# Kernel tuning notes

Measured on AMD Instinct MI355X. Metric: run time of the kernel, lower is better.

The kernel has to match this reference:

```python
import jax, jax.numpy as jnp
import numpy as np

# Static DAG configuration (mirrors GraphState): 1 input node + L layers of K nodes.
L = 8          # depth layers (well under t_budget=12)
K = 8          # nodes per layer
D = 128        # node hidden width (node.D)
B = 4096       # batch size
INDEG = 4      # in-edges per non-input node
N = 1 + L * K  # total nodes


def _build_graph():
    """Deterministic static edge lists: srcs[l][k, j] = parent node id (topologically earlier)."""
    rng = np.random.default_rng(0)
    srcs = []
    n_prev = 1  # node 0 is the INPUT node
    for _ in range(L):
        srcs.append(rng.integers(0, n_prev, size=(K, INDEG)))
        n_prev += K
    return srcs


def setup_inputs() -> dict:
    key = jax.random.key(0)
    k1, k2, k3 = jax.random.split(key, 3)
    X = jax.random.normal(k1, (B, D), dtype=jnp.float32)
    # scale ~ sqrt(2/(indeg*D)) to keep relu activations O(1) over 8 layers
    W = jax.random.normal(k2, (N, D, D), dtype=jnp.float32) * 0.06
    b = jax.random.normal(k3, (N, D), dtype=jnp.float32) * 0.01
    return {"X_batch": X, "W_all": W, "bias_all": b}


def reference(X_batch, W_all, bias_all):
    srcs = _build_graph()  # static python/numpy index constants -> jit-friendly
    # INPUT node (id 0): input_dim == D so no zero-padding; V_out = relu(X W^T + b)
    v0 = jax.nn.relu(X_batch @ W_all[0].T + bias_all[0])          # (B, D)
    outs = v0[None]                                               # (n_done, B, D)
    node = 1
    for l in range(L):
        idx = srcs[l]                                             # (K, INDEG) static
        V_in = outs[idx].sum(axis=1)                              # inbox gather-sum -> (K, B, D)
        Wl = W_all[node:node + K]                                 # (K, D, D)
        bl = bias_all[node:node + K]                              # (K, D)
        V_weighted = jnp.einsum('kbd,ked->kbe', V_in, Wl) + bl[:, None, :]
        V_out = jax.nn.relu(V_weighted)                           # apply_primitive(relu)
        outs = jnp.concatenate([outs, V_out], axis=0)
        node += K
    # output nodes = last layer; final = mean over fired output nodes
    return outs[-K:].mean(axis=0)                                 # (B, D)
```

## Files before the change

### kernel.cpp

```cpp
#include <hip/hip_runtime.h>
#include <cstdint>
#include <cstring>

#define BATCH   4096
#define DIM     128
#define NLAYERS 8
#define KNODES  8
#define NDEG    4
#define NNODES  65
#define NODE_ELEMS (BATCH * DIM)

typedef float    f32x4 __attribute__((ext_vector_type(4)));
typedef short    s16x8 __attribute__((ext_vector_type(8)));
typedef uint32_t u32x4 __attribute__((ext_vector_type(4)));

struct LayerSrcs { int p[KNODES][NDEG]; };

__device__ __forceinline__ float bf_lo(uint32_t u) {
  union { uint32_t i; float f; } x; x.i = u << 16; return x.f;
}
__device__ __forceinline__ float bf_hi(uint32_t u) {
  union { uint32_t i; float f; } x; x.i = u & 0xffff0000u; return x.f;
}
__device__ __forceinline__ uint32_t f2bf(float f) {
  union { float f; uint32_t i; } x; x.f = f;
  return (x.i + 0x7fffu + ((x.i >> 16) & 1u)) >> 16;
}
__device__ __forceinline__ uint32_t pack2(float a, float b) {
  return f2bf(a) | (f2bf(b) << 16);
}


__global__ __launch_bounds__(256)
void conv_w(const float* __restrict__ W, uint16_t* __restrict__ Wb) {
  size_t idx = ((size_t)blockIdx.x * 256 + threadIdx.x) * 8;
  f32x4 v0 = *(const f32x4*)(W + idx);
  f32x4 v1 = *(const f32x4*)(W + idx + 4);
  u32x4 pk;
  pk.x = pack2(v0.x, v0.y); pk.y = pack2(v0.z, v0.w);
  pk.z = pack2(v1.x, v1.y); pk.w = pack2(v1.z, v1.w);
  *(u32x4*)(Wb + idx) = pk;
}

template <int ROOT>
__global__ __launch_bounds__(256)
void node_gemm(const uint16_t* __restrict__ outs_r,
               uint16_t* __restrict__ outs_w,
               const uint16_t* __restrict__ Wb,
               const float* __restrict__ bias_all,
               const float* __restrict__ X,
               LayerSrcs srcs, int node_base)
{
  __shared__ char Alds[128 * 256];
  __shared__ char Blds[128 * 256];

  const int t = threadIdx.x;
  int k, tile;
  if (ROOT) { k = 0; tile = blockIdx.x; }
  else      { k = blockIdx.x & 7; tile = blockIdx.x >> 3; }
  const int node = node_base + k;
  const int row0 = tile * 128;

  const char* wsrc = (const char*)(Wb + (size_t)node * (DIM * DIM));

  const uint16_t* psrc[NDEG];
  if (!ROOT) {
#pragma unroll
    for (int p = 0; p < NDEG; ++p)
      psrc[p] = outs_r + (size_t)srcs.p[k][p] * NODE_ELEMS;
  }

#pragma unroll
  for (int it = 0; it < 8; ++it) {
    const int lin   = it * 256 + t;
    const int r     = lin >> 4;
    const int c0    = (lin & 15) << 3;
    const int lbyte = lin << 4;
    const int sbyte = lbyte ^ ((r & 7) << 4);

    float a0, a1, a2, a3, a4, a5, a6, a7;
    if (ROOT) {
      const float* xp = X + (size_t)(row0 + r) * DIM + c0;
      f32x4 v0 = *(const f32x4*)xp;
      f32x4 v1 = *(const f32x4*)(xp + 4);
      a0 = v0.x; a1 = v0.y; a2 = v0.z; a3 = v0.w;
      a4 = v1.x; a5 = v1.y; a6 = v1.z; a7 = v1.w;
    } else {
      a0 = a1 = a2 = a3 = a4 = a5 = a6 = a7 = 0.f;
#pragma unroll
      for (int p = 0; p < NDEG; ++p) {
        u32x4 v = *(const u32x4*)(psrc[p] + (size_t)(row0 + r) * DIM + c0);
        a0 += bf_lo(v.x); a1 += bf_hi(v.x);
        a2 += bf_lo(v.y); a3 += bf_hi(v.y);
        a4 += bf_lo(v.z); a5 += bf_hi(v.z);
        a6 += bf_lo(v.w); a7 += bf_hi(v.w);
      }
    }
    u32x4 pk;
    pk.x = pack2(a0, a1); pk.y = pack2(a2, a3);
    pk.z = pack2(a4, a5); pk.w = pack2(a6, a7);
    *(u32x4*)(Alds + sbyte) = pk;

    *(u32x4*)(Blds + sbyte) = *(const u32x4*)(wsrc + lbyte);
  }
  __syncthreads();

  const int lane = t & 63;
  const int w    = t >> 6;
  const int lr   = lane & 15;
  const int lg   = lane >> 4;

  f32x4 acc[2][8];
#pragma unroll
  for (int m = 0; m < 2; ++m)
#pragma unroll
    for (int n = 0; n < 8; ++n)
      acc[m][n] = (f32x4){0.f, 0.f, 0.f, 0.f};

#pragma unroll
  for (int ks = 0; ks < 4; ++ks) {
    const int kb = ks * 64 + lg * 16;
    s16x8 af[2], bfr[8];
#pragma unroll
    for (int m = 0; m < 2; ++m) {
      int r = w * 32 + m * 16 + lr;
      af[m] = *(const s16x8*)(Alds + ((r * 256 + kb) ^ ((r & 7) << 4)));
    }
#pragma unroll
    for (int n = 0; n < 8; ++n) {
      int e = n * 16 + lr;
      bfr[n] = *(const s16x8*)(Blds + ((e * 256 + kb) ^ ((e & 7) << 4)));
    }
#pragma unroll
    for (int m = 0; m < 2; ++m)
#pragma unroll
      for (int n = 0; n < 8; ++n)
        acc[m][n] = __builtin_amdgcn_mfma_f32_16x16x32_bf16(af[m], bfr[n], acc[m][n], 0, 0, 0);
  }

  uint16_t* dst = outs_w + (size_t)node * NODE_ELEMS;
  const float* bp = bias_all + (size_t)node * DIM;
#pragma unroll
  for (int n = 0; n < 8; ++n) {
    const int col = n * 16 + lr;
    const float bv = bp[col];
#pragma unroll
    for (int m = 0; m < 2; ++m) {
      const int rb = row0 + w * 32 + m * 16 + lg * 4;
#pragma unroll
      for (int j = 0; j < 4; ++j) {
        float v = fmaxf(acc[m][n][j] + bv, 0.f);
        dst[(size_t)(rb + j) * DIM + col] = (uint16_t)f2bf(v);
      }
    }
  }
}

__global__ __launch_bounds__(256)
void mean_last(const uint16_t* __restrict__ outs, float* __restrict__ out) {
  const size_t eoff = ((size_t)blockIdx.x * 256 + threadIdx.x) * 8;
  float a0 = 0, a1 = 0, a2 = 0, a3 = 0, a4 = 0, a5 = 0, a6 = 0, a7 = 0;
#pragma unroll
  for (int n = NNODES - KNODES; n < NNODES; ++n) {
    u32x4 v = *(const u32x4*)(outs + (size_t)n * NODE_ELEMS + eoff);
    a0 += bf_lo(v.x); a1 += bf_hi(v.x);
    a2 += bf_lo(v.y); a3 += bf_hi(v.y);
    a4 += bf_lo(v.z); a5 += bf_hi(v.z);
    a6 += bf_lo(v.w); a7 += bf_hi(v.w);
  }
  f32x4 o0 = {a0 * 0.125f, a1 * 0.125f, a2 * 0.125f, a3 * 0.125f};
  f32x4 o1 = {a4 * 0.125f, a5 * 0.125f, a6 * 0.125f, a7 * 0.125f};
  *(f32x4*)(out + eoff)     = o0;
  *(f32x4*)(out + eoff + 4) = o1;
}

namespace nprng {
static inline uint32_t hashmix(uint32_t v, uint32_t& hc) {
  v ^= hc; hc *= 0x931e8875u; v *= hc; v ^= v >> 16; return v;
}
static inline uint32_t mixf(uint32_t x, uint32_t y) {
  uint32_t r = x * 0xca01f9ddu - y * 0x4973f715u;
  r ^= r >> 16;
  return r;
}
struct Pcg {
  unsigned __int128 state, inc;
  bool has32; uint32_t saved;
  void step() {
    const unsigned __int128 MUL =
        ((unsigned __int128)2549297995355413924ULL << 64) | 4865540595714422341ULL;
    state = state * MUL + inc;
  }
  void init_seed0() {
    uint32_t pool[4];
    uint32_t hc = 0x43b0d7e5u;
    for (int i = 0; i < 4; ++i) pool[i] = hashmix(0u, hc);
    for (int s = 0; s < 4; ++s)
      for (int d = 0; d < 4; ++d)
        if (s != d) pool[d] = mixf(pool[d], hashmix(pool[s], hc));
    uint32_t st[8];
    uint32_t hb = 0x8b51f9ddu;
    int cyc = 0;
    for (int i = 0; i < 8; ++i) {
      uint32_t dv = pool[cyc]; cyc = (cyc + 1) & 3;
      dv ^= hb; hb *= 0x58f38dedu; dv *= hb; dv ^= dv >> 16;
      st[i] = dv;
    }
    uint64_t v[4];
    for (int i = 0; i < 4; ++i)
      v[i] = (uint64_t)st[2 * i] | ((uint64_t)st[2 * i + 1] << 32);
    unsigned __int128 s128 = ((unsigned __int128)v[0] << 64) | v[1];
    unsigned __int128 i128 = ((unsigned __int128)v[2] << 64) | v[3];
    state = 0; inc = (i128 << 1) | 1;
    step(); state += s128; step();
    has32 = false; saved = 0;
  }
  uint64_t next64() {
    step();
    uint64_t rot = (uint64_t)(state >> 122);
    uint64_t x = (uint64_t)(state >> 64) ^ (uint64_t)state;
    return rot ? ((x >> rot) | (x << (64 - rot))) : x;
  }
  uint32_t next32() {
    if (has32) { has32 = false; return saved; }
    uint64_t v = next64();
    has32 = true; saved = (uint32_t)(v >> 32);
    return (uint32_t)v;
  }
  uint32_t lemire32(uint32_t rng_incl) {
    uint32_t rng_excl = rng_incl + 1u;
    uint64_t m = (uint64_t)next32() * (uint64_t)rng_excl;
    uint32_t leftover = (uint32_t)m;
    if (leftover < rng_excl) {
      uint32_t threshold = (0xFFFFFFFFu - rng_incl) % rng_excl;
      while (leftover < threshold) {
        m = (uint64_t)next32() * (uint64_t)rng_excl;
        leftover = (uint32_t)m;
      }
    }
    return (uint32_t)(m >> 32);
  }
};
}

extern "C" void kernel_launch(void* const* d_in, const int* in_sizes, int n_in,
                              void* d_out, int out_size, void* d_ws, size_t ws_size,
                              hipStream_t stream) {
  const float* X    = (const float*)d_in[0];
  const float* W    = (const float*)d_in[1];
  const float* bias = (const float*)d_in[2];
  float* out        = (float*)d_out;

  uint16_t* Wb   = (uint16_t*)d_ws;
  uint16_t* outs = (uint16_t*)((char*)d_ws + (size_t)NNODES * DIM * DIM * 2);

  nprng::Pcg rng; rng.init_seed0();
  LayerSrcs srcs[NLAYERS];
  int n_prev = 1;
  for (int l = 0; l < NLAYERS; ++l) {
    for (int k = 0; k < KNODES; ++k)
      for (int j = 0; j < NDEG; ++j)
        srcs[l].p[k][j] = (n_prev == 1) ? 0 : (int)rng.lemire32((uint32_t)(n_prev - 1));
    n_prev += KNODES;
  }

  conv_w<<<dim3(520), dim3(256), 0, stream>>>(W, Wb);

  LayerSrcs zero{};
  node_gemm<1><<<dim3(32), dim3(256), 0, stream>>>(outs, outs, Wb, bias, X, zero, 0);

  for (int l = 0; l < NLAYERS; ++l) {
    node_gemm<0><<<dim3(256), dim3(256), 0, stream>>>(outs, outs, Wb, bias, nullptr,
                                                      srcs[l], 1 + l * KNODES);
  }

  mean_last<<<dim3(256), dim3(256), 0, stream>>>(outs, out);
}
```

Measured before the change: 138.5 us.

## Fuse whole DAG into one persistent kernel with LDS-resident node activations

Replaces the per-layer GEMM launches and the separate mean kernel with one kernel. Each block owns 16 batch rows and runs every layer, keeping live node activations in LDS slots assigned by a host-side liveness and slot allocator. The final mean is accumulated in registers. Nodes that do not reach the outputs are skipped, and weights are pre-packed into the MFMA fragment layout so they can be read straight from global memory. This removes launch overhead and the global round trips of intermediate activations. In exchange it uses a large LDS footprint (about 156KB) per block and reads weights redundantly in every block.

```diff
diff --git a/kernel.cpp b/kernel.cpp
--- a/kernel.cpp
+++ b/kernel.cpp
@@ -9,6 +9,10 @@
 #define NDEG    4
 #define NNODES  65
 #define NODE_ELEMS (BATCH * DIM)
+#define ROWS    16
+#define SLOTS   35
+#define TILE_B  (ROWS * 256)
+#define NTHREADS 512
 
 typedef float    f32x4 __attribute__((ext_vector_type(4)));
 typedef short    s16x8 __attribute__((ext_vector_type(8)));
@@ -16,6 +20,12 @@
 
 struct LayerSrcs { int p[KNODES][NDEG]; };
 
+struct Sched {
+  uint64_t pinfo[NLAYERS * KNODES];
+  int8_t   dst[NLAYERS * KNODES];
+  int8_t   root_dst;
+};
+
 __device__ __forceinline__ float bf_lo(uint32_t u) {
   union { uint32_t i; float f; } x; x.i = u << 16; return x.f;
 }
@@ -30,148 +40,211 @@
   return f2bf(a) | (f2bf(b) << 16);
 }
 
-
 __global__ __launch_bounds__(256)
-void conv_w(const float* __restrict__ W, uint16_t* __restrict__ Wb) {
-  size_t idx = ((size_t)blockIdx.x * 256 + threadIdx.x) * 8;
-  f32x4 v0 = *(const f32x4*)(W + idx);
-  f32x4 v1 = *(const f32x4*)(W + idx + 4);
+void pack_w(const float* __restrict__ W, uint16_t* __restrict__ Wp) {
+  int gid  = blockIdx.x * 256 + threadIdx.x;
+  int lane = gid & 63;
+  int n    = (gid >> 6) & 7;
+  int ks   = (gid >> 9) & 3;
+  int node = gid >> 11;
+  int col  = n * 16 + (lane & 15);
+  int k0   = ks * 32 + (lane >> 4) * 8;
+  const float* src = W + ((size_t)node * DIM + col) * DIM + k0;
+  f32x4 v0 = *(const f32x4*)src;
+  f32x4 v1 = *(const f32x4*)(src + 4);
   u32x4 pk;
   pk.x = pack2(v0.x, v0.y); pk.y = pack2(v0.z, v0.w);
   pk.z = pack2(v1.x, v1.y); pk.w = pack2(v1.z, v1.w);
-  *(u32x4*)(Wb + idx) = pk;
-}
-
-template <int ROOT>
-__global__ __launch_bounds__(256)
-void node_gemm(const uint16_t* __restrict__ outs_r,
-               uint16_t* __restrict__ outs_w,
-               const uint16_t* __restrict__ Wb,
-               const float* __restrict__ bias_all,
-               const float* __restrict__ X,
-               LayerSrcs srcs, int node_base)
+  *(u32x4*)(Wp + (size_t)gid * 8) = pk;
+}
+
+__device__ __forceinline__ void gemm_node(
+    char* lds, int sbuf, int n, int dstv,
+    const uint16_t* __restrict__ Wp, const float* __restrict__ bias,
+    uint16_t* __restrict__ outs, float* macc,
+    int row0, int lane, int w, int lr, int lg)
 {
-  __shared__ char Alds[128 * 256];
-  __shared__ char Blds[128 * 256];
-
-  const int t = threadIdx.x;
-  int k, tile;
-  if (ROOT) { k = 0; tile = blockIdx.x; }
-  else      { k = blockIdx.x & 7; tile = blockIdx.x >> 3; }
-  const int node = node_base + k;
-  const int row0 = tile * 128;
-
-  const char* wsrc = (const char*)(Wb + (size_t)node * (DIM * DIM));
-
-  const uint16_t* psrc[NDEG];
-  if (!ROOT) {
-#pragma unroll
-    for (int p = 0; p < NDEG; ++p)
-      psrc[p] = outs_r + (size_t)srcs.p[k][p] * NODE_ELEMS;
-  }
-
-#pragma unroll
-  for (int it = 0; it < 8; ++it) {
-    const int lin   = it * 256 + t;
-    const int r     = lin >> 4;
-    const int c0    = (lin & 15) << 3;
-    const int lbyte = lin << 4;
-    const int sbyte = lbyte ^ ((r & 7) << 4);
-
-    float a0, a1, a2, a3, a4, a5, a6, a7;
-    if (ROOT) {
-      const float* xp = X + (size_t)(row0 + r) * DIM + c0;
-      f32x4 v0 = *(const f32x4*)xp;
-      f32x4 v1 = *(const f32x4*)(xp + 4);
-      a0 = v0.x; a1 = v0.y; a2 = v0.z; a3 = v0.w;
-      a4 = v1.x; a5 = v1.y; a6 = v1.z; a7 = v1.w;
-    } else {
-      a0 = a1 = a2 = a3 = a4 = a5 = a6 = a7 = 0.f;
-#pragma unroll
-      for (int p = 0; p < NDEG; ++p) {
-        u32x4 v = *(const u32x4*)(psrc[p] + (size_t)(row0 + r) * DIM + c0);
-        a0 += bf_lo(v.x); a1 += bf_hi(v.x);
-        a2 += bf_lo(v.y); a3 += bf_hi(v.y);
-        a4 += bf_lo(v.z); a5 += bf_hi(v.z);
-        a6 += bf_lo(v.w); a7 += bf_hi(v.w);
-      }
-    }
-    u32x4 pk;
-    pk.x = pack2(a0, a1); pk.y = pack2(a2, a3);
-    pk.z = pack2(a4, a5); pk.w = pack2(a6, a7);
-    *(u32x4*)(Alds + sbyte) = pk;
-
-    *(u32x4*)(Blds + sbyte) = *(const u32x4*)(wsrc + lbyte);
-  }
-  __syncthreads();
-
+  if (dstv == -3) return;
+  const char* sb = lds + (size_t)(SLOTS + sbuf) * TILE_B;
+  s16x8 af[4], wf[4];
+#pragma unroll
+  for (int ks = 0; ks < 4; ++ks) {
+    af[ks] = *(const s16x8*)(sb + ((lr * 256 + ks * 64 + lg * 16) ^ ((lr & 7) << 4)));
+    wf[ks] = *(const s16x8*)(Wp + ((((size_t)n * 4 + ks) * 8 + w) << 9) + lane * 8);
+  }
+  f32x4 acc = (f32x4){0.f, 0.f, 0.f, 0.f};
+#pragma unroll
+  for (int ks = 0; ks < 4; ++ks)
+    acc = __builtin_amdgcn_mfma_f32_16x16x32_bf16(af[ks], wf[ks], acc, 0, 0, 0);
+
+  const int col = w * 16 + lr;
+  const float bv = bias[(size_t)n * DIM + col];
+  if (dstv >= 0) {
+    char* db = lds + (size_t)dstv * TILE_B;
+#pragma unroll
+    for (int j = 0; j < 4; ++j) {
+      int row = lg * 4 + j;
+      float v = fmaxf(acc[j] + bv, 0.f);
+      *(uint16_t*)(db + ((row * 256 + col * 2) ^ ((row & 7) << 4))) = (uint16_t)f2bf(v);
+    }
+  } else if (dstv == -1) {
+    uint16_t* gb = outs + (size_t)n * NODE_ELEMS + (size_t)row0 * DIM + col;
+#pragma unroll
+    for (int j = 0; j < 4; ++j) {
+      int row = lg * 4 + j;
+      float v = fmaxf(acc[j] + bv, 0.f);
+      gb[(size_t)row * DIM] = (uint16_t)f2bf(v);
+      gb += 0;
+    }
+  } else {
+#pragma unroll
+    for (int j = 0; j < 4; ++j)
+      macc[j] += 0.125f * fmaxf(acc[j] + bv, 0.f);
+  }
+}
+
+
+__device__ __forceinline__ void gemm_node2(
+    char* lds, int sbuf, int n, int dstv,
+    const uint16_t* __restrict__ Wp, const float* __restrict__ bias,
+    uint16_t* __restrict__ outs, float* macc,
+    int row0, int lane, int w, int lr, int lg)
+{
+  if (dstv == -3) return;
+  const char* sb = lds + (size_t)(SLOTS + sbuf) * TILE_B;
+  s16x8 af[4], wf[4];
+#pragma unroll
+  for (int ks = 0; ks < 4; ++ks) {
+    af[ks] = *(const s16x8*)(sb + ((lr * 256 + ks * 64 + lg * 16) ^ ((lr & 7) << 4)));
+    wf[ks] = *(const s16x8*)(Wp + ((((size_t)n * 4 + ks) * 8 + w) << 9) + lane * 8);
+  }
+  f32x4 acc = (f32x4){0.f, 0.f, 0.f, 0.f};
+#pragma unroll
+  for (int ks = 0; ks < 4; ++ks)
+    acc = __builtin_amdgcn_mfma_f32_16x16x32_bf16(af[ks], wf[ks], acc, 0, 0, 0);
+
+  const int col = w * 16 + lr;
+  const float bv = bias[(size_t)n * DIM + col];
+  if (dstv >= 0) {
+    char* db = lds + (size_t)dstv * TILE_B;
+#pragma unroll
+    for (int j = 0; j < 4; ++j) {
+      int row = lg * 4 + j;
+      float v = fmaxf(acc[j] + bv, 0.f);
+      *(uint16_t*)(db + ((row * 256 + col * 2) ^ ((row & 7) << 4))) = (uint16_t)f2bf(v);
+    }
+  } else if (dstv == -1) {
+    uint16_t* gb = outs + (size_t)n * NODE_ELEMS + (size_t)row0 * DIM + col;
+#pragma unroll
+    for (int j = 0; j < 4; ++j) {
+      int row = lg * 4 + j;
+      float v = fmaxf(acc[j] + bv, 0.f);
+      gb[(size_t)row * DIM] = (uint16_t)f2bf(v);
+    }
+  } else {
+#pragma unroll
+    for (int j = 0; j < 4; ++j)
+      macc[j] += 0.125f * fmaxf(acc[j] + bv, 0.f);
+  }
+}
+
+__global__ __launch_bounds__(NTHREADS)
+void dag_exec(const float* __restrict__ X, const uint16_t* __restrict__ Wp,
+              const float* __restrict__ bias, uint16_t* __restrict__ outs,
+              float* __restrict__ out, Sched sch)
+{
+  __shared__ char lds[(SLOTS + 4) * TILE_B];
+  const int t    = threadIdx.x;
   const int lane = t & 63;
   const int w    = t >> 6;
   const int lr   = lane & 15;
   const int lg   = lane >> 4;
-
-  f32x4 acc[2][8];
-#pragma unroll
-  for (int m = 0; m < 2; ++m)
-#pragma unroll
-    for (int n = 0; n < 8; ++n)
-      acc[m][n] = (f32x4){0.f, 0.f, 0.f, 0.f};
-
-#pragma unroll
-  for (int ks = 0; ks < 4; ++ks) {
-    const int kb = ks * 64 + lg * 16;
-    s16x8 af[2], bfr[8];
-#pragma unroll
-    for (int m = 0; m < 2; ++m) {
-      int r = w * 32 + m * 16 + lr;
-      af[m] = *(const s16x8*)(Alds + ((r * 256 + kb) ^ ((r & 7) << 4)));
-    }
-#pragma unroll
-    for (int n = 0; n < 8; ++n) {
-      int e = n * 16 + lr;
-      bfr[n] = *(const s16x8*)(Blds + ((e * 256 + kb) ^ ((e & 7) << 4)));
-    }
-#pragma unroll
-    for (int m = 0; m < 2; ++m)
-#pragma unroll
-      for (int n = 0; n < 8; ++n)
-        acc[m][n] = __builtin_amdgcn_mfma_f32_16x16x32_bf16(af[m], bfr[n], acc[m][n], 0, 0, 0);
-  }
-
-  uint16_t* dst = outs_w + (size_t)node * NODE_ELEMS;
-  const float* bp = bias_all + (size_t)node * DIM;
-#pragma unroll
-  for (int n = 0; n < 8; ++n) {
-    const int col = n * 16 + lr;
-    const float bv = bp[col];
-#pragma unroll
-    for (int m = 0; m < 2; ++m) {
-      const int rb = row0 + w * 32 + m * 16 + lg * 4;
-#pragma unroll
-      for (int j = 0; j < 4; ++j) {
-        float v = fmaxf(acc[m][n][j] + bv, 0.f);
-        dst[(size_t)(rb + j) * DIM + col] = (uint16_t)f2bf(v);
-      }
-    }
-  }
-}
-
-__global__ __launch_bounds__(256)
-void mean_last(const uint16_t* __restrict__ outs, float* __restrict__ out) {
-  const size_t eoff = ((size_t)blockIdx.x * 256 + threadIdx.x) * 8;
-  float a0 = 0, a1 = 0, a2 = 0, a3 = 0, a4 = 0, a5 = 0, a6 = 0, a7 = 0;
-#pragma unroll
-  for (int n = NNODES - KNODES; n < NNODES; ++n) {
-    u32x4 v = *(const u32x4*)(outs + (size_t)n * NODE_ELEMS + eoff);
-    a0 += bf_lo(v.x); a1 += bf_hi(v.x);
-    a2 += bf_lo(v.y); a3 += bf_hi(v.y);
-    a4 += bf_lo(v.z); a5 += bf_hi(v.z);
-    a6 += bf_lo(v.w); a7 += bf_hi(v.w);
-  }
-  f32x4 o0 = {a0 * 0.125f, a1 * 0.125f, a2 * 0.125f, a3 * 0.125f};
-  f32x4 o1 = {a4 * 0.125f, a5 * 0.125f, a6 * 0.125f, a7 * 0.125f};
-  *(f32x4*)(out + eoff)     = o0;
-  *(f32x4*)(out + eoff + 4) = o1;
+  const int row0 = blockIdx.x * ROWS;
+
+  float macc[4] = {0.f, 0.f, 0.f, 0.f};
+
+  if (t < ROWS * 16) {
+    int r = t >> 4, c = t & 15;
+    const float* xp = X + (size_t)(row0 + r) * DIM + c * 8;
+    f32x4 v0 = *(const f32x4*)xp;
+    f32x4 v1 = *(const f32x4*)(xp + 4);
+    u32x4 pk;
+    pk.x = pack2(v0.x, v0.y); pk.y = pack2(v0.z, v0.w);
+    pk.z = pack2(v1.x, v1.y); pk.w = pack2(v1.z, v1.w);
+    int off = (r * 256 + c * 16) ^ ((r & 7) << 4);
+    *(u32x4*)(lds + (size_t)SLOTS * TILE_B + off) = pk;
+  }
+  __syncthreads();
+  gemm_node2(lds, 0, 0, sch.root_dst, Wp, bias, outs, macc, row0, lane, w, lr, lg);
+  __syncthreads();
+
+  for (int l = 0; l < NLAYERS; ++l) {
+#pragma unroll
+    for (int h = 0; h < 2; ++h) {
+      const int k0 = h * 4;
+      const uint64_t pi0 = sch.pinfo[l * KNODES + k0 + 0];
+      const uint64_t pi1 = sch.pinfo[l * KNODES + k0 + 1];
+      const uint64_t pi2 = sch.pinfo[l * KNODES + k0 + 2];
+      const uint64_t pi3 = sch.pinfo[l * KNODES + k0 + 3];
+      const int d0 = sch.dst[l * KNODES + k0 + 0];
+      const int d1 = sch.dst[l * KNODES + k0 + 1];
+      const int d2 = sch.dst[l * KNODES + k0 + 2];
+      const int d3 = sch.dst[l * KNODES + k0 + 3];
+
+#pragma unroll
+      for (int it = 0; it < 2; ++it) {
+        const int lin = it * NTHREADS + t;
+        const int nk  = lin >> 8;
+        const uint64_t pinfo = (nk < 2) ? (nk == 0 ? pi0 : pi1) : (nk == 2 ? pi2 : pi3);
+        const int dv         = (nk < 2) ? (nk == 0 ? d0 : d1) : (nk == 2 ? d2 : d3);
+        if (dv != -3) {
+          const int r = (lin >> 4) & 15, c = lin & 15;
+          const int linoff = r * 256 + (c << 4);
+          const int soff   = linoff ^ ((r & 7) << 4);
+          float s0 = 0, s1 = 0, s2 = 0, s3 = 0, s4 = 0, s5 = 0, s6 = 0, s7 = 0;
+#pragma unroll
+          for (int p = 0; p < NDEG; ++p) {
+            const int e  = (int)((pinfo >> (p * 16)) & 0xffff);
+            const int ps = (e & 0xff) - 1;
+            u32x4 v;
+            if (ps >= 0) {
+              v = *(const u32x4*)(lds + (size_t)ps * TILE_B + soff);
+            } else {
+              const int pid = e >> 8;
+              v = *(const u32x4*)((const char*)(outs + (size_t)pid * NODE_ELEMS +
+                                                (size_t)row0 * DIM) + linoff);
+            }
+            s0 += bf_lo(v.x); s1 += bf_hi(v.x);
+            s2 += bf_lo(v.y); s3 += bf_hi(v.y);
+            s4 += bf_lo(v.z); s5 += bf_hi(v.z);
+            s6 += bf_lo(v.w); s7 += bf_hi(v.w);
+          }
+          u32x4 pk;
+          pk.x = pack2(s0, s1); pk.y = pack2(s2, s3);
+          pk.z = pack2(s4, s5); pk.w = pack2(s6, s7);
+          *(u32x4*)(lds + (size_t)(SLOTS + nk) * TILE_B + soff) = pk;
+        }
+      }
+      __syncthreads();
+
+#pragma unroll
+      for (int nk = 0; nk < 4; ++nk) {
+        const int dv = (nk < 2) ? (nk == 0 ? d0 : d1) : (nk == 2 ? d2 : d3);
+        const int n  = 1 + l * KNODES + k0 + nk;
+        gemm_node2(lds, nk, n, dv, Wp, bias, outs, macc, row0, lane, w, lr, lg);
+      }
+      __syncthreads();
+    }
+  }
+
+  {
+    const int col = w * 16 + lr;
+#pragma unroll
+    for (int j = 0; j < 4; ++j) {
+      const int row = lg * 4 + j;
+      out[(size_t)(row0 + row) * DIM + col] = macc[j];
+    }
+  }
 }
 
 namespace nprng {
@@ -251,7 +324,7 @@
   const float* bias = (const float*)d_in[2];
   float* out        = (float*)d_out;
 
-  uint16_t* Wb   = (uint16_t*)d_ws;
+  uint16_t* Wp   = (uint16_t*)d_ws;
   uint16_t* outs = (uint16_t*)((char*)d_ws + (size_t)NNODES * DIM * DIM * 2);
 
   nprng::Pcg rng; rng.init_seed0();
@@ -264,15 +337,58 @@
     n_prev += KNODES;
   }
 
-  conv_w<<<dim3(520), dim3(256), 0, stream>>>(W, Wb);
-
-  LayerSrcs zero{};
-  node_gemm<1><<<dim3(32), dim3(256), 0, stream>>>(outs, outs, Wb, bias, X, zero, 0);
+  bool alive[NNODES];
+  for (int i = 0; i < NNODES; ++i) alive[i] = false;
+  for (int i = NNODES - KNODES; i < NNODES; ++i) alive[i] = true;
+  for (int l = NLAYERS - 1; l >= 0; --l)
+    for (int k = 0; k < KNODES; ++k)
+      if (alive[1 + l * KNODES + k])
+        for (int j = 0; j < NDEG; ++j) alive[srcs[l].p[k][j]] = true;
+
+  int last_use[NNODES];
+  for (int i = 0; i < NNODES; ++i) last_use[i] = -1;
+  for (int l = 0; l < NLAYERS; ++l)
+    for (int k = 0; k < KNODES; ++k)
+      if (alive[1 + l * KNODES + k])
+        for (int j = 0; j < NDEG; ++j) {
+          int s = srcs[l].p[k][j];
+          if (l > last_use[s]) last_use[s] = l;
+        }
+
+  int slot_of[NNODES];
+  for (int i = 0; i < NNODES; ++i) slot_of[i] = -1;
+  int freeStk[SLOTS], nfree = 0;
+  for (int i = SLOTS - 1; i >= 0; --i) freeStk[nfree++] = i;
+
+  Sched sch;
+  slot_of[0] = freeStk[--nfree];
+  sch.root_dst = (int8_t)slot_of[0];
 
   for (int l = 0; l < NLAYERS; ++l) {
-    node_gemm<0><<<dim3(256), dim3(256), 0, stream>>>(outs, outs, Wb, bias, nullptr,
-                                                      srcs[l], 1 + l * KNODES);
-  }
-
-  mean_last<<<dim3(256), dim3(256), 0, stream>>>(outs, out);
-}
+    for (int k = 0; k < KNODES; ++k) {
+      const int node = 1 + l * KNODES + k;
+      int dv;
+      if (!alive[node])            dv = -3;
+      else if (l == NLAYERS - 1)   dv = -2;
+      else if (nfree > 0)          dv = slot_of[node] = freeStk[--nfree];
+      else                         dv = -1;
+      sch.dst[l * KNODES + k] = (int8_t)dv;
+
+      uint64_t w64 = 0;
+      for (int j = 0; j < NDEG; ++j) {
+        const int src = srcs[l].p[k][j];
+        const int enc = ((slot_of[src] + 1) & 0xff) | (src << 8);
+        w64 |= (uint64_t)enc << (j * 16);
+      }
+      sch.pinfo[l * KNODES + k] = w64;
+    }
+    for (int n = 0; n < NNODES; ++n)
+      if (slot_of[n] >= 0 && last_use[n] == l) {
+        freeStk[nfree++] = slot_of[n];
+        slot_of[n] = -1;
+      }
+  }
+
+  pack_w<<<dim3(520), dim3(256), 0, stream>>>(W, Wp);
+  dag_exec<<<dim3(BATCH / ROWS), dim3(NTHREADS), 0, stream>>>(X, Wp, bias, outs, out, sch);
+}
```

Measured after the change: 125.6 us. 1.1x faster.
